# Optimization experiments

Measured on AMD Instinct MI355X. Metric: run time of the kernel, lower is better.

The kernel has to match this reference:

```python
import jax, jax.numpy as jnp
import numpy as np

HD, M = 4096, 14336

def setup_inputs() -> dict:
    key = jax.random.key(0)
    k_x, k_g, k_u, k_d = jax.random.split(key, 4)
    scale = 1.0 / np.sqrt(HD)
    x = jax.random.normal(k_x, (4, 2048, HD), dtype=jnp.float16)
    # Dequantized fp16 weights, stored torch-style as [out_features, in_features]
    W_gate = (jax.random.normal(k_g, (M, HD), dtype=jnp.float16) * jnp.float16(scale))
    W_up   = (jax.random.normal(k_u, (M, HD), dtype=jnp.float16) * jnp.float16(scale))
    W_down = (jax.random.normal(k_d, (HD, M), dtype=jnp.float16) * jnp.float16(1.0 / np.sqrt(M)))
    return {"x": x, "W_gate": W_gate, "W_up": W_up, "W_down": W_down}

def reference(x, W_gate, W_up, W_down):
    # SwiGLU: down( silu(x @ Wg^T) * (x @ Wu^T) )
    gate = jnp.einsum("bsh,mh->bsm", x, W_gate)   # [B,S,M]
    up = jnp.einsum("bsh,mh->bsm", x, W_up)       # [B,S,M]
    h = jax.nn.silu(gate) * up                       # fused elementwise
    out = jnp.einsum("bsm,hm->bsh", h, W_down)    # [B,S,HD]
    return out
```

## Files before the change

kernel.cpp:

```cpp
#include <hip/hip_runtime.h>

typedef _Float16 f16;
typedef _Float16 f16x8 __attribute__((ext_vector_type(8)));
typedef float f32x4 __attribute__((ext_vector_type(4)));

__device__ __forceinline__ f16x8 cvt8(f32x4 lo, f32x4 hi) {
    f16x8 h;
    h[0] = (f16)lo[0]; h[1] = (f16)lo[1]; h[2] = (f16)lo[2]; h[3] = (f16)lo[3];
    h[4] = (f16)hi[0]; h[5] = (f16)hi[1]; h[6] = (f16)hi[2]; h[7] = (f16)hi[3];
    return h;
}

__global__ __launch_bounds__(256)
void cvt_f32_f16(const float* __restrict__ in, f16* __restrict__ out, long long n) {
    long long i = ((long long)blockIdx.x * 256 + threadIdx.x) * 8;
    const long long stride = (long long)gridDim.x * 256 * 8;
    for (; i < n; i += stride) {
        f32x4 a = *(const f32x4*)(in + i);
        f32x4 b = *(const f32x4*)(in + i + 4);
        *(f16x8*)(out + i) = cvt8(a, b);
    }
}

__global__ __launch_bounds__(256)
void cvt_interleave_f32_f16(const float* __restrict__ Wg,
                            const float* __restrict__ Wu,
                            f16* __restrict__ out, long long total) {
    long long i = ((long long)blockIdx.x * 256 + threadIdx.x) * 8;
    const long long stride = (long long)gridDim.x * 256 * 8;
    for (; i < total; i += stride) {
        const long long row = i >> 12;
        const int col = (int)(i & 4095);
        const long long srow = ((row >> 5) << 4) | (row & 15);
        const float* src = ((row & 16) ? Wu : Wg) + srow * 4096 + col;
        *(f16x8*)(out + i) = cvt8(*(const f32x4*)src, *(const f32x4*)(src + 4));
    }
}

__global__ void fill_sentinel_f32(float* __restrict__ out, long long n) {
    long long i = (long long)blockIdx.x * blockDim.x + threadIdx.x;
    long long stride = (long long)gridDim.x * blockDim.x;
    for (; i < n; i += stride) out[i] = 1.0f;
}

__device__ __forceinline__ void gload_lds16(const f16* g, f16* l) {
    __builtin_amdgcn_global_load_lds(
        (const __attribute__((address_space(1))) unsigned int*)(unsigned long long)g,
        (__attribute__((address_space(3))) unsigned int*)(unsigned int)(unsigned long long)l,
        16, 0, 0);
}

template<int EPI>
__global__ __launch_bounds__(512, 2)
void mlp_gemm16d(const f16* __restrict__ A, const f16* __restrict__ B0,
                 void* __restrict__ Cv, int K, int ldc,
                 int nRow, int nCol, int RG) {
    __shared__ __align__(16) f16 smA[3][256 * 32];
    __shared__ __align__(16) f16 smB0[3][256 * 32];

    const int lin   = blockIdx.x;
    const int perSg = RG * nCol;
    const int sg    = lin / perSg;
    const int rem   = lin - sg * perSg;
    int rgIn = nRow - sg * RG; if (rgIn > RG) rgIn = RG;
    const int colB = rem / rgIn;
    const int rowB = sg * RG + (rem - colB * rgIn);

    const long long blockRow = (long long)rowB * 256;
    const long long blockCol = (long long)colB * 256;

    const int tid  = threadIdx.x;
    const int w    = tid >> 6;
    const int lane = tid & 63;
    const int waveM = w >> 2;
    const int waveN = w & 3;

    const int dr   = tid >> 2;
    const int dblk = tid & 3;
    const int gblk = (dblk - (dr >> 1)) & 3;
    const f16* gA0  = A  + (blockRow + dr) * (long long)K + gblk * 8;
    const f16* gA1  = gA0 + 128 * (long long)K;
    const f16* gB0a = B0 + (blockCol + dr) * (long long)K + gblk * 8;
    const f16* gB0b = gB0a + 128 * (long long)K;
    const int wbase = w * 512;

    const int fr = lane & 15;
    const int hi = lane >> 4;
    int aOff[8], bOff[4];
#pragma unroll
    for (int i = 0; i < 8; ++i) {
        const int r = waveM * 128 + i * 16 + fr;
        aOff[i] = r * 32 + (((hi + (r >> 1)) & 3) << 3);
    }
#pragma unroll
    for (int n = 0; n < 4; ++n) {
        const int r = waveN * 64 + n * 16 + fr;
        bOff[n] = r * 32 + (((hi + (r >> 1)) & 3) << 3);
    }

    f32x4 acc0[8][4];
#pragma unroll
    for (int mi = 0; mi < 8; ++mi)
#pragma unroll
        for (int ni = 0; ni < 4; ++ni)
            acc0[mi][ni] = (f32x4){0.f, 0.f, 0.f, 0.f};

    auto stage = [&](int b) {
        gload_lds16(gA0,  &smA[b][wbase]);           gA0  += 32;
        gload_lds16(gA1,  &smA[b][4096 + wbase]);    gA1  += 32;
        gload_lds16(gB0a, &smB0[b][wbase]);          gB0a += 32;
        gload_lds16(gB0b, &smB0[b][4096 + wbase]);   gB0b += 32;
    };

    auto compute = [&](int b) {
        f16x8 aF[8], bF[4];
#pragma unroll
        for (int i = 0; i < 8; ++i) aF[i] = *(const f16x8*)(&smA[b][aOff[i]]);
#pragma unroll
        for (int n = 0; n < 4; ++n) bF[n] = *(const f16x8*)(&smB0[b][bOff[n]]);
#pragma unroll
        for (int mi = 0; mi < 8; ++mi)
#pragma unroll
            for (int ni = 0; ni < 4; ++ni)
                acc0[mi][ni] = __builtin_amdgcn_mfma_f32_16x16x32_f16(
                    aF[mi], bF[ni], acc0[mi][ni], 0, 0, 0);
    };

    const int nk = K >> 5;
    stage(0);
    stage(1);
    int cur = 0;
    for (int t = 0; t < nk - 1; ++t) {
        asm volatile("s_waitcnt vmcnt(4)" ::: "memory");
        __builtin_amdgcn_s_barrier();
        __builtin_amdgcn_sched_barrier(0);
        if (t + 2 < nk) {
            int nb = cur + 2; if (nb >= 3) nb -= 3;
            stage(nb);
        }
        compute(cur);
        cur = (cur == 2) ? 0 : cur + 1;
    }
    asm volatile("s_waitcnt vmcnt(0)" ::: "memory");
    __builtin_amdgcn_s_barrier();
    __builtin_amdgcn_sched_barrier(0);
    compute(cur);

    const long long orBase = blockRow + waveM * 128 + hi * 4;
    if constexpr (EPI == 0) {
        const long long ocBase = blockCol + waveN * 64 + fr;
#pragma unroll
        for (int mi = 0; mi < 8; ++mi)
#pragma unroll
            for (int ni = 0; ni < 4; ++ni)
#pragma unroll
                for (int j = 0; j < 4; ++j) {
                    const long long idx =
                        (orBase + mi * 16 + j) * (long long)ldc +
                        (ocBase + ni * 16);
                    ((float*)Cv)[idx] = acc0[mi][ni][j];
                }
    } else {
        const long long ocBase = (blockCol >> 1) + waveN * 32 + fr;
#pragma unroll
        for (int mi = 0; mi < 8; ++mi)
#pragma unroll
            for (int pi = 0; pi < 2; ++pi)
#pragma unroll
                for (int j = 0; j < 4; ++j) {
                    float g = acc0[mi][2 * pi][j];
                    float u = acc0[mi][2 * pi + 1][j];
                    float v = (g / (1.f + __expf(-g))) * u;
                    const long long idx =
                        (orBase + mi * 16 + j) * (long long)ldc +
                        (ocBase + pi * 16);
                    ((f16*)Cv)[idx] = (f16)v;
                }
    }
}

template<bool IS16>
__device__ __forceinline__ f16x8 load8(const char* p) {
    if constexpr (IS16) return *(const f16x8*)p;
    const float* f = (const float*)p;
    return cvt8(*(const f32x4*)f, *(const f32x4*)(f + 4));
}

template<bool FUSED, bool A16, bool B16>
__global__ __launch_bounds__(256)
void mlp_gemm(const void* __restrict__ Av, const void* __restrict__ B0v,
              const void* __restrict__ B1v, void* __restrict__ Cv,
              int K, int ldc, int nRow, int nCol, int RG) {
    __shared__ __align__(16) f16 smA[128 * 32];
    __shared__ __align__(16) f16 smB0[128 * 32];
    __shared__ __align__(16) f16 smB1[FUSED ? 128 * 32 : 8];

    const int lin   = blockIdx.x;
    const int perSg = RG * nCol;
    const int sg    = lin / perSg;
    const int rem   = lin - sg * perSg;
    int rgIn = nRow - sg * RG; if (rgIn > RG) rgIn = RG;
    const int colB = rem / rgIn;
    const int rowB = sg * RG + (rem - colB * rgIn);

    const long long blockRow = (long long)rowB * 128;
    const long long blockCol = (long long)colB * 128;

    const int tid  = threadIdx.x;
    const int w    = tid >> 6;
    const int lane = tid & 63;
    const int waveM = w >> 1;
    const int waveN = w & 1;

    const int r0 = tid >> 2;
    const int s0 = tid & 3;
    const int szA = A16 ? 2 : 4;
    const int szB = B16 ? 2 : 4;
    const char* gA0  = (const char*)Av  + ((blockRow + r0)      * (long long)K + s0 * 8) * szA;
    const char* gA1  = (const char*)Av  + ((blockRow + r0 + 64) * (long long)K + s0 * 8) * szA;
    const char* gB00 = (const char*)B0v + ((blockCol + r0)      * (long long)K + s0 * 8) * szB;
    const char* gB01 = (const char*)B0v + ((blockCol + r0 + 64) * (long long)K + s0 * 8) * szB;
    const char* gB10 = FUSED ? (const char*)B1v + ((blockCol + r0)      * (long long)K + s0 * 8) * szB : nullptr;
    const char* gB11 = FUSED ? (const char*)B1v + ((blockCol + r0 + 64) * (long long)K + s0 * 8) * szB : nullptr;

    const int off0 = tid * 8;
    const int off1 = off0 + 2048;

    const int fr = lane & 15;
    const int fk = (lane >> 4) * 8;
    int offA[4], offB[4];
#pragma unroll
    for (int i = 0; i < 4; ++i) {
        offA[i] = (waveM * 64 + i * 16 + fr) * 32 + fk;
        offB[i] = (waveN * 64 + i * 16 + fr) * 32 + fk;
    }

    f32x4 acc0[4][4];
    f32x4 acc1[4][4];
#pragma unroll
    for (int mi = 0; mi < 4; ++mi)
#pragma unroll
        for (int ni = 0; ni < 4; ++ni) {
            acc0[mi][ni] = (f32x4){0.f, 0.f, 0.f, 0.f};
            if constexpr (FUSED) acc1[mi][ni] = (f32x4){0.f, 0.f, 0.f, 0.f};
        }

    const int ksteps = K >> 5;
    for (int kt = 0; kt < ksteps; ++kt) {
        f16x8 vA0  = load8<A16>(gA0);
        f16x8 vA1  = load8<A16>(gA1);
        f16x8 vB00 = load8<B16>(gB00);
        f16x8 vB01 = load8<B16>(gB01);
        f16x8 vB10, vB11;
        if constexpr (FUSED) {
            vB10 = load8<B16>(gB10);
            vB11 = load8<B16>(gB11);
        }
        gA0 += 32 * szA; gA1 += 32 * szA;
        gB00 += 32 * szB; gB01 += 32 * szB;
        if constexpr (FUSED) { gB10 += 32 * szB; gB11 += 32 * szB; }

        __syncthreads();

        *(f16x8*)(smA  + off0) = vA0;
        *(f16x8*)(smA  + off1) = vA1;
        *(f16x8*)(smB0 + off0) = vB00;
        *(f16x8*)(smB0 + off1) = vB01;
        if constexpr (FUSED) {
            *(f16x8*)(smB1 + off0) = vB10;
            *(f16x8*)(smB1 + off1) = vB11;
        }

        __syncthreads();

        f16x8 aF[4], bF[4], b1F[4];
#pragma unroll
        for (int i = 0; i < 4; ++i) aF[i] = *(const f16x8*)(smA + offA[i]);
#pragma unroll
        for (int i = 0; i < 4; ++i) bF[i] = *(const f16x8*)(smB0 + offB[i]);
        if constexpr (FUSED) {
#pragma unroll
            for (int i = 0; i < 4; ++i) b1F[i] = *(const f16x8*)(smB1 + offB[i]);
        }

#pragma unroll
        for (int mi = 0; mi < 4; ++mi)
#pragma unroll
            for (int ni = 0; ni < 4; ++ni) {
                acc0[mi][ni] = __builtin_amdgcn_mfma_f32_16x16x32_f16(
                    aF[mi], bF[ni], acc0[mi][ni], 0, 0, 0);
                if constexpr (FUSED)
                    acc1[mi][ni] = __builtin_amdgcn_mfma_f32_16x16x32_f16(
                        aF[mi], b1F[ni], acc1[mi][ni], 0, 0, 0);
            }
    }

    const long long orBase = blockRow + waveM * 64 + ((lane >> 4) * 4);
    const long long ocBase = blockCol + waveN * 64 + fr;
#pragma unroll
    for (int mi = 0; mi < 4; ++mi)
#pragma unroll
        for (int ni = 0; ni < 4; ++ni)
#pragma unroll
            for (int j = 0; j < 4; ++j) {
                const long long idx =
                    (orBase + mi * 16 + j) * (long long)ldc + (ocBase + ni * 16);
                if constexpr (FUSED) {
                    float gv = acc0[mi][ni][j];
                    float uv = acc1[mi][ni][j];
                    float v = (gv / (1.f + __expf(-gv))) * uv;
                    ((f16*)Cv)[idx] = (f16)v;
                } else {
                    ((float*)Cv)[idx] = acc0[mi][ni][j];
                }
            }
}

extern "C" void kernel_launch(void* const* d_in, const int* in_sizes, int n_in,
                              void* d_out, int out_size, void* d_ws, size_t ws_size,
                              hipStream_t stream) {
    const float* x  = (const float*)d_in[0];
    const float* Wg = (const float*)d_in[1];
    const float* Wu = (const float*)d_in[2];
    const float* Wd = (const float*)d_in[3];
    float* out = (float*)d_out;

    const int HD = 4096;
    const int T  = in_sizes[0] / HD;
    const int M  = in_sizes[1] / HD;

    const long long nW = (long long)M * HD;
    const long long nX = (long long)T * HD;
    const size_t wBytes = (size_t)nW * 2;
    const size_t xBytes = (size_t)nX * 2;
    const size_t hRow   = (size_t)M * 2;
    const size_t minH   = 256 * hRow;

    char* p = (char*)d_ws;
    size_t rem = ws_size;
    f16 *Wgu = nullptr, *Wd16 = nullptr, *X16 = nullptr;
    bool fast = false;
    if (rem >= 3 * wBytes + xBytes + minH) {
        Wgu  = (f16*)p; p += 2 * wBytes;
        Wd16 = (f16*)p; p += wBytes;
        X16  = (f16*)p; p += xBytes;
        rem -= 3 * wBytes + xBytes;
        fast = true;
    }
    f16* H = (f16*)p;

    if (fast) {
        long long maxRows = (long long)(rem / hRow);
        int chunk = (int)((maxRows / 256) * 256);
        if (chunk > T) chunk = T;

        cvt_interleave_f32_f16<<<2048, 256, 0, stream>>>(Wg, Wu, Wgu, 2 * nW);
        cvt_f32_f16<<<2048, 256, 0, stream>>>(Wd, Wd16, nW);
        cvt_f32_f16<<<2048, 256, 0, stream>>>(x, X16, nX);

        const int nColGU = (2 * M) / 256;
        const int nColD  = HD / 256;
        for (int t0 = 0; t0 < T; t0 += chunk) {
            int rows = (T - t0 < chunk) ? (T - t0) : chunk;
            int nRow = rows / 256;
            mlp_gemm16d<3><<<dim3(nRow * nColGU), 512, 0, stream>>>(
                X16 + (size_t)t0 * HD, Wgu, H, HD, M, nRow, nColGU, nRow);
            int RG = (nRow < 16) ? nRow : 16;
            mlp_gemm16d<0><<<dim3(nRow * nColD), 512, 0, stream>>>(
                H, Wd16, out + (size_t)t0 * HD, M, HD, nRow, nColD, RG);
        }
        return;
    }

    long long maxRows = (long long)(ws_size / hRow);
    int chunk = (int)((maxRows / 128) * 128);
    if (chunk > T) chunk = T;
    if (chunk <= 0) {
        fill_sentinel_f32<<<1024, 256, 0, stream>>>(out, (long long)out_size);
        return;
    }
    f16* Hf = (f16*)d_ws;
    for (int t0 = 0; t0 < T; t0 += chunk) {
        int rows = (T - t0 < chunk) ? (T - t0) : chunk;
        int nRow = rows / 128;
        {
            int nCol = M / 128;
            mlp_gemm<true, false, false><<<dim3(nRow * nCol), 256, 0, stream>>>(
                x + (size_t)t0 * HD, Wg, Wu, Hf, HD, M, nRow, nCol, nRow);
        }
        {
            int nCol = HD / 128;
            int RG = (nRow < 32) ? nRow : 32;
            mlp_gemm<false, true, false><<<dim3(nRow * nCol), 256, 0, stream>>>(
                Hf, Wd, nullptr, out + (size_t)t0 * HD, M, HD, nRow, nCol, RG);
        }
    }
}
```

Measured before the change: 2.758 ms.

## Restructure GEMM main loop into 8-wave ping-pong with priority-phased MFMA blocks

Replaces the triple-buffered 32-wide K loop with a double-buffered 64-wide K step split into four phases. Each phase loads LDS fragments, issues part of the next global-to-LDS prefetch, then runs a 4x4 MFMA block at raised wave priority between barriers. The intent is to interleave memory and matrix work across the two co-resident workgroups and waves, keeping the MFMA units busy more of the time. It adds barriers per K step and uses somewhat more LDS, and its correctness depends on the hand-tuned vmcnt waits matching the prefetch order.

```diff
diff --git a/kernel.cpp b/kernel.cpp
--- a/kernel.cpp
+++ b/kernel.cpp
@@ -50,13 +50,24 @@
         16, 0, 0);
 }
 
+__device__ __forceinline__ void phase_pre() {
+    __builtin_amdgcn_s_barrier();
+    asm volatile("s_waitcnt lgkmcnt(0)" ::: "memory");
+    __builtin_amdgcn_sched_barrier(0);
+    __builtin_amdgcn_s_setprio(1);
+}
+__device__ __forceinline__ void phase_post() {
+    __builtin_amdgcn_s_setprio(0);
+    __builtin_amdgcn_s_barrier();
+}
+
 template<int EPI>
 __global__ __launch_bounds__(512, 2)
-void mlp_gemm16d(const f16* __restrict__ A, const f16* __restrict__ B0,
-                 void* __restrict__ Cv, int K, int ldc,
-                 int nRow, int nCol, int RG) {
-    __shared__ __align__(16) f16 smA[3][256 * 32];
-    __shared__ __align__(16) f16 smB0[3][256 * 32];
+void mlp_gemm8p(const f16* __restrict__ A, const f16* __restrict__ B0,
+                void* __restrict__ Cv, int K, int ldc,
+                int nRow, int nCol, int RG) {
+    __shared__ __align__(16) f16 smA[2][2][256 * 32];
+    __shared__ __align__(16) f16 smB[2][2][256 * 32];
 
     const int lin   = blockIdx.x;
     const int perSg = RG * nCol;
@@ -78,11 +89,20 @@
     const int dr   = tid >> 2;
     const int dblk = tid & 3;
     const int gblk = (dblk - (dr >> 1)) & 3;
-    const f16* gA0  = A  + (blockRow + dr) * (long long)K + gblk * 8;
-    const f16* gA1  = gA0 + 128 * (long long)K;
-    const f16* gB0a = B0 + (blockCol + dr) * (long long)K + gblk * 8;
-    const f16* gB0b = gB0a + 128 * (long long)K;
+    const f16* gA0 = A  + (blockRow + dr) * (long long)K + gblk * 8;
+    const f16* gA1 = gA0 + 128 * (long long)K;
+    const f16* gB0 = B0 + (blockCol + dr) * (long long)K + gblk * 8;
+    const f16* gB1 = gB0 + 128 * (long long)K;
     const int wbase = w * 512;
+
+    auto stageA = [&](int b, int ks) {
+        gload_lds16(gA0, &smA[b][ks][wbase]);        gA0 += 32;
+        gload_lds16(gA1, &smA[b][ks][4096 + wbase]); gA1 += 32;
+    };
+    auto stageB = [&](int b, int ks) {
+        gload_lds16(gB0, &smB[b][ks][wbase]);        gB0 += 32;
+        gload_lds16(gB1, &smB[b][ks][4096 + wbase]); gB1 += 32;
+    };
 
     const int fr = lane & 15;
     const int hi = lane >> 4;
@@ -98,53 +118,84 @@
         bOff[n] = r * 32 + (((hi + (r >> 1)) & 3) << 3);
     }
 
-    f32x4 acc0[8][4];
+    f32x4 acc[8][4];
 #pragma unroll
     for (int mi = 0; mi < 8; ++mi)
 #pragma unroll
         for (int ni = 0; ni < 4; ++ni)
-            acc0[mi][ni] = (f32x4){0.f, 0.f, 0.f, 0.f};
-
-    auto stage = [&](int b) {
-        gload_lds16(gA0,  &smA[b][wbase]);           gA0  += 32;
-        gload_lds16(gA1,  &smA[b][4096 + wbase]);    gA1  += 32;
-        gload_lds16(gB0a, &smB0[b][wbase]);          gB0a += 32;
-        gload_lds16(gB0b, &smB0[b][4096 + wbase]);   gB0b += 32;
-    };
-
-    auto compute = [&](int b) {
-        f16x8 aF[8], bF[4];
-#pragma unroll
-        for (int i = 0; i < 8; ++i) aF[i] = *(const f16x8*)(&smA[b][aOff[i]]);
-#pragma unroll
-        for (int n = 0; n < 4; ++n) bF[n] = *(const f16x8*)(&smB0[b][bOff[n]]);
-#pragma unroll
-        for (int mi = 0; mi < 8; ++mi)
-#pragma unroll
-            for (int ni = 0; ni < 4; ++ni)
-                acc0[mi][ni] = __builtin_amdgcn_mfma_f32_16x16x32_f16(
-                    aF[mi], bF[ni], acc0[mi][ni], 0, 0, 0);
-    };
-
-    const int nk = K >> 5;
-    stage(0);
-    stage(1);
-    int cur = 0;
-    for (int t = 0; t < nk - 1; ++t) {
-        asm volatile("s_waitcnt vmcnt(4)" ::: "memory");
+            acc[mi][ni] = (f32x4){0.f, 0.f, 0.f, 0.f};
+
+    const int nk2 = K >> 6;
+
+    stageA(0, 0); stageB(0, 0);
+    stageA(0, 1); stageB(0, 1);
+    stageA(1, 0); stageB(1, 0);
+    stageB(1, 1);
+    asm volatile("s_waitcnt vmcnt(6)" ::: "memory");
+    __builtin_amdgcn_s_barrier();
+
+    for (int t = 0; t < nk2; ++t) {
+        const int c = t & 1;
+        f16x8 aF[4], bF0[4], bF1[4];
+
+#pragma unroll
+        for (int i = 0; i < 4; ++i) aF[i]  = *(const f16x8*)(&smA[c][0][aOff[i]]);
+#pragma unroll
+        for (int n = 0; n < 4; ++n) bF0[n] = *(const f16x8*)(&smB[c][0][bOff[n]]);
+        if (t + 1 < nk2) stageA(c ^ 1, 1);
+        phase_pre();
+#pragma unroll
+        for (int i = 0; i < 4; ++i)
+#pragma unroll
+            for (int n = 0; n < 4; ++n)
+                acc[i][n] = __builtin_amdgcn_mfma_f32_16x16x32_f16(
+                    aF[i], bF0[n], acc[i][n], 0, 0, 0);
+        phase_post();
+
+#pragma unroll
+        for (int i = 0; i < 4; ++i) aF[i] = *(const f16x8*)(&smA[c][0][aOff[4 + i]]);
+        if (t + 2 < nk2) stageB(c, 0);
+        phase_pre();
+#pragma unroll
+        for (int i = 0; i < 4; ++i)
+#pragma unroll
+            for (int n = 0; n < 4; ++n)
+                acc[4 + i][n] = __builtin_amdgcn_mfma_f32_16x16x32_f16(
+                    aF[i], bF0[n], acc[4 + i][n], 0, 0, 0);
+        phase_post();
+
+#pragma unroll
+        for (int i = 0; i < 4; ++i) aF[i]  = *(const f16x8*)(&smA[c][1][aOff[i]]);
+#pragma unroll
+        for (int n = 0; n < 4; ++n) bF1[n] = *(const f16x8*)(&smB[c][1][bOff[n]]);
+        if (t + 2 < nk2) stageA(c, 0);
+        phase_pre();
+#pragma unroll
+        for (int i = 0; i < 4; ++i)
+#pragma unroll
+            for (int n = 0; n < 4; ++n)
+                acc[i][n] = __builtin_amdgcn_mfma_f32_16x16x32_f16(
+                    aF[i], bF1[n], acc[i][n], 0, 0, 0);
+        phase_post();
+
+#pragma unroll
+        for (int i = 0; i < 4; ++i) aF[i] = *(const f16x8*)(&smA[c][1][aOff[4 + i]]);
+        if (t + 2 < nk2) stageB(c, 1);
+        phase_pre();
+#pragma unroll
+        for (int i = 0; i < 4; ++i)
+#pragma unroll
+            for (int n = 0; n < 4; ++n)
+                acc[4 + i][n] = __builtin_amdgcn_mfma_f32_16x16x32_f16(
+                    aF[i], bF1[n], acc[4 + i][n], 0, 0, 0);
+        __builtin_amdgcn_s_setprio(0);
+        if (t + 2 < nk2) {
+            asm volatile("s_waitcnt vmcnt(6)" ::: "memory");
+        } else {
+            asm volatile("s_waitcnt vmcnt(0)" ::: "memory");
+        }
         __builtin_amdgcn_s_barrier();
-        __builtin_amdgcn_sched_barrier(0);
-        if (t + 2 < nk) {
-            int nb = cur + 2; if (nb >= 3) nb -= 3;
-            stage(nb);
-        }
-        compute(cur);
-        cur = (cur == 2) ? 0 : cur + 1;
-    }
-    asm volatile("s_waitcnt vmcnt(0)" ::: "memory");
-    __builtin_amdgcn_s_barrier();
-    __builtin_amdgcn_sched_barrier(0);
-    compute(cur);
+    }
 
     const long long orBase = blockRow + waveM * 128 + hi * 4;
     if constexpr (EPI == 0) {
@@ -158,7 +209,7 @@
                     const long long idx =
                         (orBase + mi * 16 + j) * (long long)ldc +
                         (ocBase + ni * 16);
-                    ((float*)Cv)[idx] = acc0[mi][ni][j];
+                    ((float*)Cv)[idx] = acc[mi][ni][j];
                 }
     } else {
         const long long ocBase = (blockCol >> 1) + waveN * 32 + fr;
@@ -168,8 +219,8 @@
             for (int pi = 0; pi < 2; ++pi)
 #pragma unroll
                 for (int j = 0; j < 4; ++j) {
-                    float g = acc0[mi][2 * pi][j];
-                    float u = acc0[mi][2 * pi + 1][j];
+                    float g = acc[mi][2 * pi][j];
+                    float u = acc[mi][2 * pi + 1][j];
                     float v = (g / (1.f + __expf(-g))) * u;
                     const long long idx =
                         (orBase + mi * 16 + j) * (long long)ldc +
@@ -363,10 +414,10 @@
         for (int t0 = 0; t0 < T; t0 += chunk) {
             int rows = (T - t0 < chunk) ? (T - t0) : chunk;
             int nRow = rows / 256;
-            mlp_gemm16d<3><<<dim3(nRow * nColGU), 512, 0, stream>>>(
+            mlp_gemm8p<3><<<dim3(nRow * nColGU), 512, 0, stream>>>(
                 X16 + (size_t)t0 * HD, Wgu, H, HD, M, nRow, nColGU, nRow);
             int RG = (nRow < 16) ? nRow : 16;
-            mlp_gemm16d<0><<<dim3(nRow * nColD), 512, 0, stream>>>(
+            mlp_gemm8p<0><<<dim3(nRow * nColD), 512, 0, stream>>>(
                 H, Wd16, out + (size_t)t0 * HD, M, HD, nRow, nColD, RG);
         }
         return;
```

Result: no change. 2.806 ms (+1.7%).
